# Kernel tuning notes

Hardware: AMD Instinct MI355X
Metric: run time of the kernel (lower is better)

The kernel has to match this reference:

```python
import jax, jax.numpy as jnp
import numpy as np
import math

FACIL_RATE = 2.0
FIRE_THRESH = 0.85
MAX_GATE = 8.0
N_BUF = 512
TOP_K_FRAC = 0.1
B, T, D = 4, 4096, 2048


def _gelu(x):
    c = math.sqrt(2.0 / math.pi)
    return 0.5 * x * (1.0 + jnp.tanh(c * (x + 0.044715 * x * x * x)))


def setup_inputs() -> dict:
    key = jax.random.key(0)
    k1, k2, k3 = jax.random.split(key, 3)
    x = jax.random.normal(k1, (B, T, D), dtype=jnp.float32)
    log_strength = jnp.asarray(0.0, dtype=jnp.float32)
    # Steady-state ring buffer: keys = normalized mean vectors, masks = top-k(|mean|) indicators
    means = jax.random.normal(k2, (N_BUF, D), dtype=jnp.float32)
    buf_keys = means / jnp.linalg.norm(means, axis=-1, keepdims=True)
    top_k = max(1, int(D * TOP_K_FRAC))  # 204
    _, top_idx = jax.lax.top_k(jnp.abs(means), top_k)  # (N_BUF, top_k)
    buf_masks = jnp.zeros((N_BUF, D), dtype=jnp.float32).at[
        jnp.arange(N_BUF)[:, None], top_idx].set(1.0)
    facil = 1.0 + 3.0 * jax.random.uniform(k3, (N_BUF,), dtype=jnp.float32)
    valid_mask = jnp.ones((N_BUF,), dtype=bool)
    return {"x": x, "log_strength": log_strength, "buf_keys": buf_keys,
            "buf_masks": buf_masks, "facil": facil, "valid_mask": valid_mask}


def reference(x, log_strength, buf_keys, buf_masks, facil, valid_mask):
    # Steady-state (pass1_complete) path of GELU277.forward
    y = _gelu(x)  # (B, T, D)
    # m_curr = y.detach().flatten(0,1).mean(0)  -> stop_gradient as in torch no_grad
    m_curr = jax.lax.stop_gradient(y).reshape(-1, y.shape[-1]).mean(0)  # (D,)
    q = m_curr / jnp.linalg.norm(m_curr)
    sims = buf_keys @ q                      # (N_BUF,) cosine similarities
    sims = jnp.where(valid_mask, sims, -1.0)
    nearest = jnp.argmax(sims)
    sim_max = sims[nearest]
    # facil[nearest] *= FACIL_RATE if fired, then read (.item() in torch -> constant)
    f = jax.lax.stop_gradient(facil[nearest]) * jnp.where(sim_max > FIRE_THRESH, FACIL_RATE, 1.0)
    # strength.item() in torch -> no grad through log_strength
    strength = jax.lax.stop_gradient(jnp.clip(jnp.exp(log_strength), 0.01, 5.0))
    k_amp = jnp.minimum(1.0 + strength * (f - 1.0), MAX_GATE)
    topk_mask = jax.lax.stop_gradient(buf_masks[nearest])  # (D,)
    gate = 1.0 + (k_amp - 1.0) * topk_mask
    return y * gate[None, None, :]
```

## Files before the change

kernel.cpp:

```cpp
#include <hip/hip_runtime.h>
#include <math.h>

#define DCOLS 2048
#define NROWS 16384
#define NBUF  512
#define NB_PART 512

__device__ __forceinline__ float gelu_f(float x) {
    const float c = 0.7978845608028654f;
    float u = c * (x + 0.044715f * x * x * x);
    float e = __expf(2.0f * u);
    float t = 1.0f - 2.0f / (1.0f + e);
    return 0.5f * x * (1.0f + t);
}

__global__ __launch_bounds__(512) void k_colsum_part(const float* __restrict__ x,
                                                     float* __restrict__ part) {
    int t = threadIdx.x;
    int col = t * 4;
    float a0 = 0.f, a1 = 0.f, a2 = 0.f, a3 = 0.f;
    for (int r = blockIdx.x; r < NROWS; r += gridDim.x) {
        float4 v = *reinterpret_cast<const float4*>(x + (size_t)r * DCOLS + col);
        a0 += gelu_f(v.x); a1 += gelu_f(v.y); a2 += gelu_f(v.z); a3 += gelu_f(v.w);
    }
    float4 st; st.x = a0; st.y = a1; st.z = a2; st.w = a3;
    *reinterpret_cast<float4*>(part + (size_t)blockIdx.x * DCOLS + col) = st;
}

__global__ __launch_bounds__(512) void k_colsum_atomic(const float* __restrict__ x,
                                                       float* __restrict__ colsum) {
    int t = threadIdx.x;
    int col = t * 4;
    float a0 = 0.f, a1 = 0.f, a2 = 0.f, a3 = 0.f;
    for (int r = blockIdx.x; r < NROWS; r += gridDim.x) {
        float4 v = *reinterpret_cast<const float4*>(x + (size_t)r * DCOLS + col);
        a0 += gelu_f(v.x); a1 += gelu_f(v.y); a2 += gelu_f(v.z); a3 += gelu_f(v.w);
    }
    atomicAdd(&colsum[col + 0], a0);
    atomicAdd(&colsum[col + 1], a1);
    atomicAdd(&colsum[col + 2], a2);
    atomicAdd(&colsum[col + 3], a3);
}

__global__ __launch_bounds__(256) void k_colsum_reduce(const float* __restrict__ part,
                                                       float* __restrict__ colsum) {
    int col = blockIdx.x * blockDim.x + threadIdx.x;
    float a = 0.f;
    for (int b = 0; b < NB_PART; ++b)
        a += part[(size_t)b * DCOLS + col];
    colsum[col] = a;
}

__global__ __launch_bounds__(64) void k_sims(const float* __restrict__ keys,
                                             const float* __restrict__ colsum,
                                             float* __restrict__ s) {
    int row = blockIdx.x;
    int lane = threadIdx.x;
    const float* kr = keys + (size_t)row * DCOLS;
    float acc = 0.f;
    for (int j = lane * 4; j < DCOLS; j += 64 * 4) {
        float4 kv = *reinterpret_cast<const float4*>(kr + j);
        float4 cv = *reinterpret_cast<const float4*>(colsum + j);
        acc += kv.x * cv.x + kv.y * cv.y + kv.z * cv.z + kv.w * cv.w;
    }
    for (int off = 32; off; off >>= 1) acc += __shfl_down(acc, off);
    if (lane == 0) s[row] = acc;
}

__global__ __launch_bounds__(256) void k_gate(const float* __restrict__ colsum,
                                              const float* __restrict__ s,
                                              const float* __restrict__ log_strength,
                                              const float* __restrict__ facil,
                                              const float* __restrict__ masks,
                                              float* __restrict__ gate) {
    __shared__ float red[256];
    __shared__ int   redi[256];
    int t = threadIdx.x;

    float n2 = 0.f;
    for (int j = t; j < DCOLS; j += 256) { float v = colsum[j]; n2 += v * v; }
    red[t] = n2; __syncthreads();
    for (int off = 128; off; off >>= 1) {
        if (t < off) red[t] += red[t + off];
        __syncthreads();
    }
    float norm = sqrtf(red[0]);
    __syncthreads();

    float best = -1e30f; int bi = 0x7fffffff;
    for (int j = t; j < NBUF; j += 256) {
        float v = s[j];
        if (v > best || (v == best && j < bi)) { best = v; bi = j; }
    }
    red[t] = best; redi[t] = bi; __syncthreads();
    for (int off = 128; off; off >>= 1) {
        if (t < off) {
            float ov = red[t + off]; int oi = redi[t + off];
            if (ov > red[t] || (ov == red[t] && oi < redi[t])) { red[t] = ov; redi[t] = oi; }
        }
        __syncthreads();
    }
    int nearest = redi[0];
    float sim_max = red[0] / norm;

    float strength = __expf(log_strength[0]);
    strength = fminf(fmaxf(strength, 0.01f), 5.0f);
    float f = facil[nearest] * (sim_max > 0.85f ? 2.0f : 1.0f);
    float k_amp = fminf(1.0f + strength * (f - 1.0f), 8.0f);

    const float* mrow = masks + (size_t)nearest * DCOLS;
    for (int j = t; j < DCOLS; j += 256)
        gate[j] = 1.0f + (k_amp - 1.0f) * mrow[j];
}

__global__ __launch_bounds__(512) void k_scale(const float* __restrict__ x,
                                               const float* __restrict__ gate,
                                               float* __restrict__ out) {
    int t = threadIdx.x;
    int col = t * 4;
    float4 g = *reinterpret_cast<const float4*>(gate + col);
    for (int r = blockIdx.x; r < NROWS; r += gridDim.x) {
        size_t off = (size_t)r * DCOLS + col;
        float4 v = *reinterpret_cast<const float4*>(x + off);
        float4 o;
        o.x = gelu_f(v.x) * g.x;
        o.y = gelu_f(v.y) * g.y;
        o.z = gelu_f(v.z) * g.z;
        o.w = gelu_f(v.w) * g.w;
        *reinterpret_cast<float4*>(out + off) = o;
    }
}

extern "C" void kernel_launch(void* const* d_in, const int* in_sizes, int n_in,
                              void* d_out, int out_size, void* d_ws, size_t ws_size,
                              hipStream_t stream) {
    const float* x            = (const float*)d_in[0];
    const float* log_strength = (const float*)d_in[1];
    const float* keys         = (const float*)d_in[2];
    const float* masks        = (const float*)d_in[3];
    const float* facil        = (const float*)d_in[4];
    float* out = (float*)d_out;
    float* ws  = (float*)d_ws;

    float* colsum = ws;
    float* s      = ws + 2048;
    float* gate   = ws + 2560;
    float* part   = ws + 4608;

    size_t need_part = (size_t)(4608 + (size_t)NB_PART * DCOLS) * sizeof(float);

    if (ws_size >= need_part) {
        k_colsum_part<<<NB_PART, 512, 0, stream>>>(x, part);
        k_colsum_reduce<<<DCOLS / 256, 256, 0, stream>>>(part, colsum);
    } else {
        hipMemsetAsync(colsum, 0, DCOLS * sizeof(float), stream);
        k_colsum_atomic<<<NB_PART, 512, 0, stream>>>(x, colsum);
    }
    k_sims<<<NBUF, 64, 0, stream>>>(keys, colsum, s);
    k_gate<<<1, 256, 0, stream>>>(colsum, s, log_strength, facil, masks, gate);
    k_scale<<<1024, 512, 0, stream>>>(x, gate, out);
}
```

Measured before the change: 111.2 us.

## Parallelize partial reduction, widen sims/scale kernels, use nontemporal output stores

The column-sum reduce is split across a 2D grid of 64-partial chunks, and the chunks are combined with atomics into a zeroed colsum. When workspace allows, the partial pass uses 1024 blocks. The sims kernel uses 256 threads per key row with a single load per thread and a cross-wave reduction. The scale kernel processes 8 floats per thread with nontemporal stores to avoid polluting cache. Together these aim to cut the serial 512-deep reduce and improve occupancy, at the cost of an extra memset and atomics that make the summation order nondeterministic.

```diff
diff --git a/kernel.cpp b/kernel.cpp
--- a/kernel.cpp
+++ b/kernel.cpp
@@ -4,7 +4,8 @@
 #define DCOLS 2048
 #define NROWS 16384
 #define NBUF  512
-#define NB_PART 512
+
+typedef float v4f __attribute__((ext_vector_type(4)));
 
 __device__ __forceinline__ float gelu_f(float x) {
     const float c = 0.7978845608028654f;
@@ -44,27 +45,33 @@
 
 __global__ __launch_bounds__(256) void k_colsum_reduce(const float* __restrict__ part,
                                                        float* __restrict__ colsum) {
-    int col = blockIdx.x * blockDim.x + threadIdx.x;
+    int col = blockIdx.x * 256 + threadIdx.x;
+    int base = blockIdx.y * 64;
     float a = 0.f;
-    for (int b = 0; b < NB_PART; ++b)
-        a += part[(size_t)b * DCOLS + col];
-    colsum[col] = a;
+#pragma unroll 8
+    for (int b = 0; b < 64; ++b)
+        a += part[(size_t)(base + b) * DCOLS + col];
+    atomicAdd(&colsum[col], a);
 }
 
-__global__ __launch_bounds__(64) void k_sims(const float* __restrict__ keys,
-                                             const float* __restrict__ colsum,
-                                             float* __restrict__ s) {
+__global__ __launch_bounds__(256) void k_sims(const float* __restrict__ keys,
+                                              const float* __restrict__ colsum,
+                                              float* __restrict__ s) {
+    __shared__ float wsum[4];
     int row = blockIdx.x;
-    int lane = threadIdx.x;
+    int t = threadIdx.x;
     const float* kr = keys + (size_t)row * DCOLS;
-    float acc = 0.f;
-    for (int j = lane * 4; j < DCOLS; j += 64 * 4) {
-        float4 kv = *reinterpret_cast<const float4*>(kr + j);
-        float4 cv = *reinterpret_cast<const float4*>(colsum + j);
-        acc += kv.x * cv.x + kv.y * cv.y + kv.z * cv.z + kv.w * cv.w;
-    }
+    int j = t * 8;
+    float4 k0 = *reinterpret_cast<const float4*>(kr + j);
+    float4 k1 = *reinterpret_cast<const float4*>(kr + j + 4);
+    float4 c0 = *reinterpret_cast<const float4*>(colsum + j);
+    float4 c1 = *reinterpret_cast<const float4*>(colsum + j + 4);
+    float acc = k0.x * c0.x + k0.y * c0.y + k0.z * c0.z + k0.w * c0.w
+              + k1.x * c1.x + k1.y * c1.y + k1.z * c1.z + k1.w * c1.w;
     for (int off = 32; off; off >>= 1) acc += __shfl_down(acc, off);
-    if (lane == 0) s[row] = acc;
+    if ((t & 63) == 0) wsum[t >> 6] = acc;
+    __syncthreads();
+    if (t == 0) s[row] = wsum[0] + wsum[1] + wsum[2] + wsum[3];
 }
 
 __global__ __launch_bounds__(256) void k_gate(const float* __restrict__ colsum,
@@ -113,21 +120,28 @@
         gate[j] = 1.0f + (k_amp - 1.0f) * mrow[j];
 }
 
-__global__ __launch_bounds__(512) void k_scale(const float* __restrict__ x,
+__global__ __launch_bounds__(256) void k_scale(const float* __restrict__ x,
                                                const float* __restrict__ gate,
                                                float* __restrict__ out) {
     int t = threadIdx.x;
-    int col = t * 4;
-    float4 g = *reinterpret_cast<const float4*>(gate + col);
+    int col = t * 8;
+    float4 g0 = *reinterpret_cast<const float4*>(gate + col);
+    float4 g1 = *reinterpret_cast<const float4*>(gate + col + 4);
     for (int r = blockIdx.x; r < NROWS; r += gridDim.x) {
         size_t off = (size_t)r * DCOLS + col;
-        float4 v = *reinterpret_cast<const float4*>(x + off);
-        float4 o;
-        o.x = gelu_f(v.x) * g.x;
-        o.y = gelu_f(v.y) * g.y;
-        o.z = gelu_f(v.z) * g.z;
-        o.w = gelu_f(v.w) * g.w;
-        *reinterpret_cast<float4*>(out + off) = o;
+        float4 v0 = *reinterpret_cast<const float4*>(x + off);
+        float4 v1 = *reinterpret_cast<const float4*>(x + off + 4);
+        v4f o0, o1;
+        o0.x = gelu_f(v0.x) * g0.x;
+        o0.y = gelu_f(v0.y) * g0.y;
+        o0.z = gelu_f(v0.z) * g0.z;
+        o0.w = gelu_f(v0.w) * g0.w;
+        o1.x = gelu_f(v1.x) * g1.x;
+        o1.y = gelu_f(v1.y) * g1.y;
+        o1.z = gelu_f(v1.z) * g1.z;
+        o1.w = gelu_f(v1.w) * g1.w;
+        __builtin_nontemporal_store(o0, reinterpret_cast<v4f*>(out + off));
+        __builtin_nontemporal_store(o1, reinterpret_cast<v4f*>(out + off + 4));
     }
 }
 
@@ -147,16 +161,24 @@
     float* gate   = ws + 2560;
     float* part   = ws + 4608;
 
-    size_t need_part = (size_t)(4608 + (size_t)NB_PART * DCOLS) * sizeof(float);
+    auto need = [](int nbp) {
+        return (size_t)(4608 + (size_t)nbp * DCOLS) * sizeof(float);
+    };
 
-    if (ws_size >= need_part) {
-        k_colsum_part<<<NB_PART, 512, 0, stream>>>(x, part);
-        k_colsum_reduce<<<DCOLS / 256, 256, 0, stream>>>(part, colsum);
+    int nbp = 0;
+    if (ws_size >= need(1024)) nbp = 1024;
+    else if (ws_size >= need(512)) nbp = 512;
+
+    (void)hipMemsetAsync(colsum, 0, DCOLS * sizeof(float), stream);
+
+    if (nbp) {
+        k_colsum_part<<<nbp, 512, 0, stream>>>(x, part);
+        dim3 rg(DCOLS / 256, nbp / 64);
+        k_colsum_reduce<<<rg, 256, 0, stream>>>(part, colsum);
     } else {
-        hipMemsetAsync(colsum, 0, DCOLS * sizeof(float), stream);
-        k_colsum_atomic<<<NB_PART, 512, 0, stream>>>(x, colsum);
+        k_colsum_atomic<<<512, 512, 0, stream>>>(x, colsum);
     }
-    k_sims<<<NBUF, 64, 0, stream>>>(keys, colsum, s);
+    k_sims<<<NBUF, 256, 0, stream>>>(keys, colsum, s);
     k_gate<<<1, 256, 0, stream>>>(colsum, s, log_strength, facil, masks, gate);
-    k_scale<<<1024, 512, 0, stream>>>(x, gate, out);
+    k_scale<<<2048, 256, 0, stream>>>(x, gate, out);
 }
```

Measured after the change: 95.41 us. 1.17x faster.
